# Kernel tuning notes

Measured on AMD Instinct MI355X. Metric: run time of the kernel, lower is better.

The kernel has to match this reference:

```python
import jax, jax.numpy as jnp
import numpy as np

B, T, D, H, L, F, V, BANDS = 16, 512, 1024, 8, 6, 4096, 30000, 16
RES = [1, 1, 2, 2, 4, 4, 8, 8]  # per-head K/V resolution schedule
HD = D // H


def setup_inputs() -> dict:
    key = jax.random.key(0)
    ks = iter(jax.random.split(key, 64))
    s = 0.02
    p = {
        "tokens": jax.random.randint(next(ks), (B, T), 0, V, dtype=jnp.int32),
        "embed": jax.random.normal(next(ks), (V, D), jnp.float32) * s,
        "pos_embed": jax.random.normal(next(ks), (T, D), jnp.float32) * s,
        "Wq": jax.random.normal(next(ks), (L, D, D), jnp.float32) * s,
        "bq": jnp.zeros((L, D), jnp.float32),
        "Wk": jax.random.normal(next(ks), (L, D, D), jnp.float32) * s,
        "bk": jnp.zeros((L, D), jnp.float32),
        "Wv": jax.random.normal(next(ks), (L, D, D), jnp.float32) * s,
        "bv": jnp.zeros((L, D), jnp.float32),
        "Wo": jax.random.normal(next(ks), (L, D, D), jnp.float32) * s,
        "bo": jnp.zeros((L, D), jnp.float32),
        "ln1_g": jnp.ones((L, D), jnp.float32),
        "ln1_b": jnp.zeros((L, D), jnp.float32),
        "ln2_g": jnp.ones((L, D), jnp.float32),
        "ln2_b": jnp.zeros((L, D), jnp.float32),
        "W1": jax.random.normal(next(ks), (L, D, F), jnp.float32) * s,
        "b1": jnp.zeros((L, F), jnp.float32),
        "W2": jax.random.normal(next(ks), (L, F, D), jnp.float32) * s,
        "b2": jnp.zeros((L, D), jnp.float32),
        "gates": jnp.ones((L, H, BANDS), jnp.float32),
        "lnf_g": jnp.ones((D,), jnp.float32),
        "lnf_b": jnp.zeros((D,), jnp.float32),
    }
    return p


def _ln(x, g, b, eps=1e-5):
    mu = jnp.mean(x, -1, keepdims=True)
    var = jnp.var(x, -1, keepdims=True)
    return (x - mu) * jax.lax.rsqrt(var + eps) * g + b


def _hfa_attention(x, Wq, bq, Wk, bk, Wv, bv, Wo, bo, gates_l):
    # x: [B,T,D]; per-head resolution schedule + spectral band gating.
    q = (x @ Wq + bq).reshape(B, T, H, HD).transpose(0, 2, 1, 3)  # [B,H,T,HD]
    k = (x @ Wk + bk).reshape(B, T, H, HD).transpose(0, 2, 1, 3)
    v = (x @ Wv + bv).reshape(B, T, H, HD).transpose(0, 2, 1, 3)
    nb = T // 2 + 1
    band_of_bin = (jnp.arange(nb) * BANDS) // nb  # map rfft bin -> spectral band
    scale = 1.0 / np.sqrt(HD)
    outs = []
    for h in range(H):
        r = RES[h]
        kh = k[:, h].reshape(B, T // r, r, HD).mean(2)  # pooled keys [B,T/r,HD]
        vh = v[:, h].reshape(B, T // r, r, HD).mean(2)
        scores = jnp.einsum("btd,bsd->bts", q[:, h], kh) * scale
        attn = jax.nn.softmax(scores, axis=-1)
        o = jnp.einsum("bts,bsd->btd", attn, vh)  # [B,T,HD]
        # spectral band gating along sequence axis
        g = gates_l[h][band_of_bin]  # [nb]
        f = jnp.fft.rfft(o, axis=1) * g[None, :, None]
        o = jnp.fft.irfft(f, n=T, axis=1)
        outs.append(o)
    out = jnp.concatenate(outs, axis=-1)  # [B,T,D]
    return out @ Wo + bo


def reference(tokens, embed, pos_embed, Wq, bq, Wk, bk, Wv, bv, Wo, bo,
              ln1_g, ln1_b, ln2_g, ln2_b, W1, b1, W2, b2, gates, lnf_g, lnf_b):
    x = embed[tokens] + pos_embed[jnp.arange(T)][None, :, :]  # [B,T,D]
    for l in range(L):
        h = _ln(x, ln1_g[l], ln1_b[l])
        x = x + _hfa_attention(h, Wq[l], bq[l], Wk[l], bk[l], Wv[l], bv[l],
                               Wo[l], bo[l], gates[l])
        h = _ln(x, ln2_g[l], ln2_b[l])
        ff = jax.nn.gelu(h @ W1[l] + b1[l], approximate=False) @ W2[l] + b2[l]
        x = x + ff
    return _ln(x, lnf_g, lnf_b)
```

## Files before the change

### kernel.cpp

```cpp
#include <hip/hip_runtime.h>
#include <hip/hip_bf16.h>
#include <math.h>

#define Bn 16
#define Tn 512
#define Dn 1024
#define Hn 8
#define Ln 6
#define Fn 4096
#define HDn 128

typedef __attribute__((ext_vector_type(8))) short short8;
typedef __attribute__((ext_vector_type(4))) float f32x4;

__device__ __forceinline__ float bf2f(unsigned short u){
  union{float f; unsigned int i;} c; c.i = ((unsigned int)u)<<16; return c.f;
}
__device__ __forceinline__ unsigned short f2bf(float f){
  union{float f; unsigned int i;} c; c.f=f;
  unsigned int r = c.i + 0x7fffu + ((c.i>>16)&1u);
  return (unsigned short)(r>>16);
}

#define GLOAD(gp, lp) __builtin_amdgcn_global_load_lds( \
    (const __attribute__((address_space(1))) void*)(const void*)(gp), \
    (__attribute__((address_space(3))) void*)(void*)(lp), 16, 0, 0)

__global__ __launch_bounds__(256) void embed_kernel(
    const int* __restrict__ tok, const float* __restrict__ emb,
    const float* __restrict__ pos, float* __restrict__ x){
  long row = blockIdx.x;
  int t = (int)(row & (Tn-1));
  int tk = tok[row];
  int d = threadIdx.x*4;
  float4 e = *(const float4*)(emb + (long)tk*Dn + d);
  float4 p = *(const float4*)(pos + (long)t*Dn + d);
  float4 r; r.x=e.x+p.x; r.y=e.y+p.y; r.z=e.z+p.z; r.w=e.w+p.w;
  *(float4*)(x + row*(long)Dn + d) = r;
}

template<int OUTBF>
__global__ __launch_bounds__(256) void ln_kernel(
    const float* __restrict__ x, const float* __restrict__ g,
    const float* __restrict__ b, void* __restrict__ outp){
  long row = blockIdx.x;
  const float* xr = x + row*(long)Dn;
  int tid = threadIdx.x;
  float4 v4 = *(const float4*)(xr + tid*4);
  float s  = v4.x+v4.y+v4.z+v4.w;
  float s2 = v4.x*v4.x + v4.y*v4.y + v4.z*v4.z + v4.w*v4.w;
  #pragma unroll
  for (int o=32;o;o>>=1){ s += __shfl_xor(s,o); s2 += __shfl_xor(s2,o); }
  __shared__ float rs[4], rs2[4];
  int w = tid>>6;
  if ((tid&63)==0){ rs[w]=s; rs2[w]=s2; }
  __syncthreads();
  s  = rs[0]+rs[1]+rs[2]+rs[3];
  s2 = rs2[0]+rs2[1]+rs2[2]+rs2[3];
  float mu  = s*(1.f/Dn);
  float var = s2*(1.f/Dn) - mu*mu;
  float rstd = rsqrtf(var + 1e-5f);
  float4 gg = *(const float4*)(g + tid*4);
  float4 bb = *(const float4*)(b + tid*4);
  float o0 = (v4.x-mu)*rstd*gg.x + bb.x;
  float o1 = (v4.y-mu)*rstd*gg.y + bb.y;
  float o2 = (v4.z-mu)*rstd*gg.z + bb.z;
  float o3 = (v4.w-mu)*rstd*gg.w + bb.w;
  if (OUTBF){
    unsigned short* o = (unsigned short*)outp + row*(long)Dn + tid*4;
    o[0]=f2bf(o0); o[1]=f2bf(o1); o[2]=f2bf(o2); o[3]=f2bf(o3);
  } else {
    float* o = (float*)outp + row*(long)Dn + tid*4;
    o[0]=o0; o[1]=o1; o[2]=o2; o[3]=o3;
  }
}

__global__ __launch_bounds__(256) void transpose_w(
    const float* __restrict__ W, unsigned short* __restrict__ WT, int Kd, int Nd){
  __shared__ float tile[32][33];
  long lofs = (long)blockIdx.z * Kd * Nd;
  int n0 = blockIdx.x*32, k0 = blockIdx.y*32;
  int tx = threadIdx.x & 31, ty = threadIdx.x >> 5;
  #pragma unroll
  for (int i=0;i<4;i++){
    int kk = k0 + ty + i*8;
    tile[ty+i*8][tx] = W[lofs + (long)kk*Nd + n0 + tx];
  }
  __syncthreads();
  #pragma unroll
  for (int i=0;i<4;i++){
    int nn = n0 + ty + i*8;
    WT[lofs + (long)nn*Kd + k0 + tx] = f2bf(tile[tx][ty+i*8]);
  }
}

__global__ __launch_bounds__(256) void pack_bias(
    const float* __restrict__ bq, const float* __restrict__ bk,
    const float* __restrict__ bv, float* __restrict__ bqkv){
  int i = blockIdx.x*256 + threadIdx.x;
  int l = i / (3*Dn); int r = i - l*3*Dn; int w = r / Dn; int d = r - w*Dn;
  const float* src = (w==0)? bq : ((w==1)? bk : bv);
  bqkv[i] = src[l*Dn + d];
}

__global__ __launch_bounds__(512) void ckern(
    const float* __restrict__ gates, float* __restrict__ cbuf){
  int lh = blockIdx.x;
  __shared__ float gb[16];
  if (threadIdx.x < 16) gb[threadIdx.x] = gates[lh*16 + threadIdx.x];
  __syncthreads();
  int m = threadIdx.x;
  float acc = gb[0];
  for (int j=1;j<256;j++){
    int band = (j*16)/257;
    int kmod = (j*m) & 511;
    acc += 2.f*gb[band]*cosf(1.2271846303085129e-2f * (float)kmod);
  }
  acc += gb[15] * ((m & 1) ? -1.f : 1.f);
  cbuf[lh*512 + m] = acc * (1.f/512.f);
}

__global__ __launch_bounds__(256) void gfill(
    const float* __restrict__ cbuf, unsigned short* __restrict__ G){
  long idx = (long)blockIdx.x*256 + threadIdx.x;
  int lh = (int)(idx >> 18);
  int rem = (int)(idx & 262143);
  int t = rem >> 9, s = rem & 511;
  G[idx] = f2bf(cbuf[lh*512 + ((t - s) & 511)]);
}

__global__ __launch_bounds__(256) void pool_kernel(
    const unsigned short* __restrict__ kin, const unsigned short* __restrict__ vin,
    unsigned short* __restrict__ kp, unsigned short* __restrict__ vTp){
  long idx = (long)blockIdx.x*256 + threadIdx.x;
  if (idx >= (long)Bn*1920*HDn) return;
  long rem = idx; int hh = 0; int S = 512;
  for (hh=0; hh<8; hh++){
    S = 512 >> (hh>>1);
    long seg = (long)Bn*S*HDn;
    if (rem < seg) break;
    rem -= seg;
  }
  int r = 512 / S;
  int d = (int)(rem % HDn);
  long t2 = rem / HDn;
  int s = (int)(t2 % S);
  int b = (int)(t2 / S);
  const unsigned short* kb = kin + ((long)(b*Tn + s*r))*Dn + hh*HDn + d;
  const unsigned short* vb = vin + ((long)(b*Tn + s*r))*Dn + hh*HDn + d;
  float ks=0.f, vs=0.f;
  for (int j=0;j<r;j++){ ks += bf2f(kb[(long)j*Dn]); vs += bf2f(vb[(long)j*Dn]); }
  float inv = 1.f/(float)r;
  int pref=0;
  for (int g2=0; g2<hh; g2++) pref += 512 >> (g2>>1);
  long segb = (long)Bn*HDn*pref;
  kp [segb + ((long)b*S + s)*HDn + d] = f2bf(ks*inv);
  vTp[segb + ((long)b*HDn + d)*S + s] = f2bf(vs*inv);
}

template<int S>
__global__ __launch_bounds__(256) void softmax_kernel(
    const float* __restrict__ sc, unsigned short* __restrict__ at){
  const int NV = S/64;
  long row = (long)blockIdx.x*4 + (threadIdx.x >> 6);
  const float* r = sc + row*(long)S;
  int lane = threadIdx.x & 63;
  float vals[NV];
  float mx = -1e30f;
  #pragma unroll
  for (int i=0;i<NV;i++){ vals[i] = r[lane + i*64] * 0.08838834764831845f; mx = fmaxf(mx, vals[i]); }
  #pragma unroll
  for (int o=32;o;o>>=1) mx = fmaxf(mx, __shfl_xor(mx, o));
  float sum = 0.f;
  #pragma unroll
  for (int i=0;i<NV;i++){ vals[i] = expf(vals[i]-mx); sum += vals[i]; }
  #pragma unroll
  for (int o=32;o;o>>=1) sum += __shfl_xor(sum, o);
  float inv = 1.f/sum;
  #pragma unroll
  for (int i=0;i<NV;i++) at[row*(long)S + lane + i*64] = f2bf(vals[i]*inv);
}

template<int MODE>
__global__ __launch_bounds__(256)
void gemm_kernel(const unsigned short* __restrict__ A, int lda, long sAb, long sAh,
                 const unsigned short* __restrict__ Bt, int ldb, long sBb, long sBh,
                 void* __restrict__ Cout, int ldc, long sCb, long sCh,
                 const float* __restrict__ bias, long sbias,
                 int zshift, int zmask,
                 int M, int N, int K)
{
  __shared__ unsigned short AB[2][2][128*64];
  int z = blockIdx.z;
  int zb = z & zmask, zh = z >> zshift;
  const unsigned short* Az = A + (long)zb*sAb + (long)zh*sAh;
  const unsigned short* Bz = Bt + (long)zb*sBb + (long)zh*sBh;
  const float* biasz = bias ? (bias + (long)zh*sbias) : nullptr;
  int m0 = blockIdx.y*128, n0 = blockIdx.x*128;
  int tid = threadIdx.x;
  int lane = tid & 63, wid = tid >> 6;
  int wm = wid >> 1, wn = wid & 1;
  f32x4 zero4 = {0.f,0.f,0.f,0.f};
  f32x4 acc[4][4];
  #pragma unroll
  for (int m=0;m<4;m++)
    #pragma unroll
    for (int n=0;n<4;n++)
      acc[m][n] = zero4;
  const int r16 = lane & 15, kq = lane >> 4;

  auto stage = [&](int buf, int k0){
    #pragma unroll
    for (int i=0;i<4;i++){
      int chunk = i*256 + tid;
      int row = chunk >> 3, c = chunk & 7;
      int cg = (c ^ (row & 7)) * 8;
      int gm = m0 + row; gm = gm < M ? gm : M-1;
      GLOAD(Az + (long)gm*lda + k0 + cg, AB[buf][0] + (i*256 + wid*64)*8);
    }
    #pragma unroll
    for (int i=0;i<4;i++){
      int chunk = i*256 + tid;
      int row = chunk >> 3, c = chunk & 7;
      int cg = (c ^ (row & 7)) * 8;
      int gn = n0 + row; gn = gn < N ? gn : N-1;
      GLOAD(Bz + (long)gn*ldb + k0 + cg, AB[buf][1] + (i*256 + wid*64)*8);
    }
  };

  int NT = K >> 6;
  stage(0, 0);
  for (int t = 0; t < NT; t++){
    if (t + 1 < NT){
      stage((t+1)&1, (t+1)*64);
      asm volatile("s_waitcnt vmcnt(8)" ::: "memory");
    } else {
      asm volatile("s_waitcnt vmcnt(0)" ::: "memory");
    }
    __builtin_amdgcn_s_barrier();
    const unsigned short* As = AB[t&1][0];
    const unsigned short* Bs = AB[t&1][1];
    #pragma unroll
    for (int kk=0; kk<64; kk+=32){
      short8 af[4], bfr[4];
      int kb = (kk + kq*8) * 2;
      #pragma unroll
      for (int m=0;m<4;m++){
        int row = wm*64 + m*16 + r16;
        af[m] = *(const short8*)((const char*)As + row*128 + (kb ^ ((row & 7) << 4)));
      }
      #pragma unroll
      for (int n=0;n<4;n++){
        int row = wn*64 + n*16 + r16;
        bfr[n] = *(const short8*)((const char*)Bs + row*128 + (kb ^ ((row & 7) << 4)));
      }
      #pragma unroll
      for (int m=0;m<4;m++)
        #pragma unroll
        for (int n=0;n<4;n++)
          acc[m][n] = __builtin_amdgcn_mfma_f32_16x16x32_bf16(af[m], bfr[n], acc[m][n], 0, 0, 0);
    }
    __builtin_amdgcn_s_barrier();
  }
  #pragma unroll
  for (int n=0;n<4;n++){
    int col = n0 + wn*64 + n*16 + r16;
    if (col >= N) continue;
    float bvv = 0.f;
    if (MODE != 0 && biasz != nullptr) bvv = biasz[col];
    #pragma unroll
    for (int m=0;m<4;m++){
      #pragma unroll
      for (int e=0;e<4;e++){
        int row = m0 + wm*64 + m*16 + kq*4 + e;
        if (row >= M) continue;
        float vv = acc[m][n][e] + bvv;
        long cidx = (long)zb*sCb + (long)zh*sCh + (long)row*ldc + col;
        if (MODE == 0)      ((float*)Cout)[cidx] = vv;
        else                ((unsigned short*)Cout)[cidx] = f2bf(vv);
      }
    }
  }
}

template<int MODE, int Mt, int Nt, int Kt, long SBH, long SCH, int BIASST>
__global__ __launch_bounds__(256)
void gemm_big(const unsigned short* __restrict__ A,
              const unsigned short* __restrict__ Bt,
              void* __restrict__ Cout,
              const float* __restrict__ bias)
{
  __shared__ char shraw[2][32768];
  int zh = blockIdx.z;
  const unsigned short* Bz = Bt + (long)zh*SBH;
  const float* biasz = bias + (long)zh*BIASST;
  int m0 = blockIdx.y*128, n0 = blockIdx.x*128;
  int tid = threadIdx.x;
  int lane = tid & 63, wid = tid >> 6;
  int wm = wid >> 1, wn = wid & 1;
  f32x4 zero4 = {0.f,0.f,0.f,0.f};
  f32x4 acc[4][4];
  #pragma unroll
  for (int m=0;m<4;m++)
    #pragma unroll
    for (int n=0;n<4;n++)
      acc[m][n] = zero4;
  const int r16 = lane & 15, kq = lane >> 4;

  const unsigned short* pA[4];
  const unsigned short* pB[4];
  #pragma unroll
  for (int i=0;i<4;i++){
    int chunk = i*256 + tid;
    int row = chunk >> 3, c = chunk & 7;
    int cg = (c ^ (row & 7)) * 8;
    pA[i] = A  + (long)(m0 + row)*Kt + cg;
    pB[i] = Bz + (long)(n0 + row)*Kt + cg;
  }
  auto stage = [&](int buf, int k0){
    unsigned short* As = (unsigned short*)shraw[buf];
    #pragma unroll
    for (int i=0;i<4;i++) GLOAD(pA[i] + k0, As + (i*256 + wid*64)*8);
    #pragma unroll
    for (int i=0;i<4;i++) GLOAD(pB[i] + k0, As + 8192 + (i*256 + wid*64)*8);
  };

  constexpr int NT = Kt/64;
  stage(0, 0);
  for (int t = 0; t < NT; t++){
    if (t + 1 < NT){
      stage((t+1)&1, (t+1)*64);
      asm volatile("s_waitcnt vmcnt(8)" ::: "memory");
    } else {
      asm volatile("s_waitcnt vmcnt(0)" ::: "memory");
    }
    __builtin_amdgcn_s_barrier();
    const unsigned short* As = (const unsigned short*)shraw[t&1];
    const unsigned short* Bs = As + 8192;
    #pragma unroll
    for (int kk=0; kk<64; kk+=32){
      short8 af[4], bfr[4];
      int kb = (kk + kq*8) * 2;
      #pragma unroll
      for (int m=0;m<4;m++){
        int row = wm*64 + m*16 + r16;
        af[m] = *(const short8*)((const char*)As + row*128 + (kb ^ ((row & 7) << 4)));
      }
      #pragma unroll
      for (int n=0;n<4;n++){
        int row = wn*64 + n*16 + r16;
        bfr[n] = *(const short8*)((const char*)Bs + row*128 + (kb ^ ((row & 7) << 4)));
      }
      #pragma unroll
      for (int m=0;m<4;m++)
        #pragma unroll
        for (int n=0;n<4;n++)
          acc[m][n] = __builtin_amdgcn_mfma_f32_16x16x32_bf16(af[m], bfr[n], acc[m][n], 0, 0, 0);
    }
    __builtin_amdgcn_s_barrier();
  }

  if (MODE == 1 || MODE == 2){
    unsigned short* shb = (unsigned short*)&shraw[0][0];
    #pragma unroll
    for (int n=0;n<4;n++){
      int col = wn*64 + n*16 + r16;
      float bvv = biasz[n0 + col];
      #pragma unroll
      for (int m=0;m<4;m++){
        #pragma unroll
        for (int e=0;e<4;e++){
          int row = wm*64 + m*16 + kq*4 + e;
          float vv = acc[m][n][e] + bvv;
          if (MODE == 2) vv = 0.5f*vv*(1.f + erff(vv*0.7071067811865475f));
          shb[row*136 + col] = f2bf(vv);
        }
      }
    }
    __syncthreads();
    #pragma unroll
    for (int i=0;i<8;i++){
      int chunk = i*256 + tid;
      int row = chunk >> 4, col = (chunk & 15)*8;
      short8 vv8 = *(const short8*)(shb + row*136 + col);
      *(short8*)((unsigned short*)Cout + (long)zh*SCH +
                 (long)(m0 + row)*Nt + n0 + col) = vv8;
    }
  } else {
    float* shf = (float*)&shraw[0][0];
    #pragma unroll
    for (int ph=0; ph<2; ph++){
      __syncthreads();
      if (wm == ph){
        #pragma unroll
        for (int n=0;n<4;n++){
          int col = wn*64 + n*16 + r16;
          float bvv = biasz[n0 + col];
          #pragma unroll
          for (int m=0;m<4;m++){
            #pragma unroll
            for (int e=0;e<4;e++){
              int rl = m*16 + kq*4 + e;
              shf[rl*136 + col] = acc[m][n][e] + bvv;
            }
          }
        }
      }
      __syncthreads();
      #pragma unroll
      for (int i=0;i<8;i++){
        int chunk = i*256 + tid;
        int row = chunk >> 5, col = (chunk & 31)*4;
        float4 vv = *(const float4*)(shf + row*136 + col);
        float* cp = (float*)Cout + (long)(m0 + ph*64 + row)*Nt + n0 + col;
        float4 o = *(const float4*)cp;
        o.x += vv.x; o.y += vv.y; o.z += vv.z; o.w += vv.w;
        *(float4*)cp = o;
      }
    }
  }
}

extern "C" void kernel_launch(void* const* d_in, const int* in_sizes, int n_in,
                              void* d_out, int out_size, void* d_ws, size_t ws_size,
                              hipStream_t stream){
  const int*   tokens = (const int*)  d_in[0];
  const float* embedp = (const float*)d_in[1];
  const float* pos    = (const float*)d_in[2];
  const float* Wq  = (const float*)d_in[3];
  const float* bq  = (const float*)d_in[4];
  const float* Wk  = (const float*)d_in[5];
  const float* bk  = (const float*)d_in[6];
  const float* Wv  = (const float*)d_in[7];
  const float* bv  = (const float*)d_in[8];
  const float* Wo  = (const float*)d_in[9];
  const float* bo  = (const float*)d_in[10];
  const float* ln1g= (const float*)d_in[11];
  const float* ln1b= (const float*)d_in[12];
  const float* ln2g= (const float*)d_in[13];
  const float* ln2b= (const float*)d_in[14];
  const float* W1  = (const float*)d_in[15];
  const float* b1  = (const float*)d_in[16];
  const float* W2  = (const float*)d_in[17];
  const float* b2  = (const float*)d_in[18];
  const float* gates=(const float*)d_in[19];
  const float* lnfg= (const float*)d_in[20];
  const float* lnfb= (const float*)d_in[21];
  float* out = (float*)d_out;

  char* base = (char*)d_ws;
  size_t off = 0;
  auto take = [&](size_t bytes)->char*{
    char* p = base + off;
    off = (off + bytes + 255) & ~(size_t)255;
    return p;
  };
  unsigned short* WqT = (unsigned short*)take((size_t)Ln*Dn*Dn*2);
  unsigned short* WkT = (unsigned short*)take((size_t)Ln*Dn*Dn*2);
  unsigned short* WvT = (unsigned short*)take((size_t)Ln*Dn*Dn*2);
  unsigned short* WoT = (unsigned short*)take((size_t)Ln*Dn*Dn*2);
  unsigned short* W1T = (unsigned short*)take((size_t)Ln*Dn*Fn*2);
  unsigned short* W2T = (unsigned short*)take((size_t)Ln*Dn*Fn*2);
  unsigned short* G   = (unsigned short*)take((size_t)Ln*Hn*Tn*Tn*2);
  float*          cbuf= (float*)take((size_t)Ln*Hn*Tn*4);
  float*          bqkv= (float*)take((size_t)Ln*3*Dn*4);
  float*          x   = (float*)take((size_t)Bn*Tn*Dn*4);
  unsigned short* hbuf= (unsigned short*)take((size_t)Bn*Tn*Dn*2);
  unsigned short* q   = (unsigned short*)take((size_t)Bn*Tn*Dn*2);
  unsigned short* k   = (unsigned short*)take((size_t)Bn*Tn*Dn*2);
  unsigned short* v   = (unsigned short*)take((size_t)Bn*Tn*Dn*2);
  unsigned short* kp  = (unsigned short*)take((size_t)Bn*1920*HDn*2);
  unsigned short* vTp = (unsigned short*)take((size_t)Bn*1920*HDn*2);
  unsigned short* ao  = (unsigned short*)take((size_t)Bn*Tn*Dn*2);
  unsigned short* ff1 = (unsigned short*)take((size_t)Bn*Tn*Fn*2);
  if (off > ws_size) return;
  float*          scoresA = (float*)ff1;
  unsigned short* attnA   = (unsigned short*)(scoresA + (size_t)2*Bn*Tn*512);
  unsigned short* oT = k;

  transpose_w<<<dim3(Dn/32, Dn/32, Ln), 256, 0, stream>>>(Wq, WqT, Dn, Dn);
  transpose_w<<<dim3(Dn/32, Dn/32, Ln), 256, 0, stream>>>(Wk, WkT, Dn, Dn);
  transpose_w<<<dim3(Dn/32, Dn/32, Ln), 256, 0, stream>>>(Wv, WvT, Dn, Dn);
  transpose_w<<<dim3(Dn/32, Dn/32, Ln), 256, 0, stream>>>(Wo, WoT, Dn, Dn);
  transpose_w<<<dim3(Fn/32, Dn/32, Ln), 256, 0, stream>>>(W1, W1T, Dn, Fn);
  transpose_w<<<dim3(Dn/32, Fn/32, Ln), 256, 0, stream>>>(W2, W2T, Fn, Dn);
  pack_bias<<<(Ln*3*Dn)/256, 256, 0, stream>>>(bq, bk, bv, bqkv);
  ckern<<<Ln*Hn, 512, 0, stream>>>(gates, cbuf);
  gfill<<<(Ln*Hn*Tn*Tn)/256, 256, 0, stream>>>(cbuf, G);
  embed_kernel<<<Bn*Tn, 256, 0, stream>>>(tokens, embedp, pos, x);

  const int pref[8] = {0,512,1024,1280,1536,1664,1792,1856};
  const int MT = Bn*Tn;

  for (int l=0; l<Ln; l++){
    ln_kernel<1><<<MT, 256, 0, stream>>>(x, ln1g + l*Dn, ln1b + l*Dn, hbuf);
    gemm_big<1, 8192, Dn, Dn, (long)Ln*Dn*Dn, (long)Bn*Tn*Dn, Dn>
        <<<dim3(Dn/128, MT/128, 3), 256, 0, stream>>>(
        hbuf, WqT + (size_t)l*Dn*Dn, q, bqkv + (size_t)l*3*Dn);
    pool_kernel<<<((long)Bn*1920*HDn + 255)/256, 256, 0, stream>>>(k, v, kp, vTp);

    for (int g=0; g<4; g++){
      int h0 = 2*g;
      int S  = Tn >> g;
      long koff = (long)Bn*HDn*pref[h0];
      gemm_kernel<0><<<dim3((S+127)/128, Tn/128, 32), 256, 0, stream>>>(
          q + h0*HDn, Dn, (long)Tn*Dn, (long)HDn,
          kp + koff, HDn, (long)S*HDn, (long)Bn*HDn*S,
          scoresA, S, (long)Tn*S, (long)Bn*Tn*S,
          nullptr, 0L, 4, 15,
          Tn, S, HDn);
      switch (S){
        case 512: softmax_kernel<512><<<2*MT/4, 256, 0, stream>>>(scoresA, attnA); break;
        case 256: softmax_kernel<256><<<2*MT/4, 256, 0, stream>>>(scoresA, attnA); break;
        case 128: softmax_kernel<128><<<2*MT/4, 256, 0, stream>>>(scoresA, attnA); break;
        default:  softmax_kernel< 64><<<2*MT/4, 256, 0, stream>>>(scoresA, attnA); break;
      }
      gemm_kernel<1><<<dim3(Tn/128, HDn/128, 32), 256, 0, stream>>>(
          vTp + koff, S, (long)HDn*S, (long)Bn*HDn*S,
          attnA, S, (long)Tn*S, (long)Bn*Tn*S,
          oT + (size_t)h0*Bn*HDn*Tn, Tn, (long)HDn*Tn, (long)Bn*HDn*Tn,
          nullptr, 0L, 4, 15,
          HDn, Tn, S);
    }
    gemm_kernel<1><<<dim3(1, Tn/128, 128), 256, 0, stream>>>(
        G + (size_t)(l*Hn)*Tn*Tn, Tn, 0L, (long)Tn*Tn,
        oT, Tn, (long)HDn*Tn, (long)Bn*HDn*Tn,
        ao, Dn, (long)Tn*Dn, (long)HDn,
        nullptr, 0L, 4, 15,
        Tn, HDn, Tn);
    gemm_big<3, 8192, Dn, Dn, 0L, 0L, 0>
        <<<dim3(Dn/128, MT/128, 1), 256, 0, stream>>>(
        ao, WoT + (size_t)l*Dn*Dn, x, bo + l*Dn);
    ln_kernel<1><<<MT, 256, 0, stream>>>(x, ln2g + l*Dn, ln2b + l*Dn, hbuf);
    gemm_big<2, 8192, Fn, Dn, 0L, 0L, 0>
        <<<dim3(Fn/128, MT/128, 1), 256, 0, stream>>>(
        hbuf, W1T + (size_t)l*Dn*Fn, ff1, b1 + l*Fn);
    gemm_big<3, 8192, Dn, Fn, 0L, 0L, 0>
        <<<dim3(Dn/128, MT/128, 1), 256, 0, stream>>>(
        ff1, W2T + (size_t)l*Dn*Fn, x, b2 + l*Dn);
  }
  ln_kernel<0><<<MT, 256, 0, stream>>>(x, lnfg, lnfb, out);
}
```

Measured before the change: 3.118 ms.

## Batch all attention head groups into single scores, softmax and PV launches

Replaces the per-resolution-group loop of twelve launches (scores GEMM, softmax, PV GEMM for each of four groups) with three launches covering all eight heads. Each kernel derives its head's pooled length and buffer offset from blockIdx. Scores and attention probabilities are packed for all heads, with attention getting its own workspace allocation. Block-level work is now unbalanced across heads: blocks for short heads exit early or loop fewer K tiles. Scores blocks use a fixed 128-wide tile even when the pooled length is 64. The aim is to cut launch and tail overhead and fill the GPU better for the small-S heads.

```diff
diff --git a/kernel.cpp b/kernel.cpp
--- a/kernel.cpp
+++ b/kernel.cpp
@@ -20,6 +20,10 @@
   union{float f; unsigned int i;} c; c.f=f;
   unsigned int r = c.i + 0x7fffu + ((c.i>>16)&1u);
   return (unsigned short)(r>>16);
+}
+__device__ __forceinline__ int pref_of(int h){
+  int g = h >> 1;
+  return (2048 - (2048 >> g)) + (h & 1) * (512 >> g);
 }
 
 #define GLOAD(gp, lp) __builtin_amdgcn_global_load_lds( \
@@ -158,27 +162,38 @@
   vTp[segb + ((long)b*HDn + d)*S + s] = f2bf(vs*inv);
 }
 
-template<int S>
-__global__ __launch_bounds__(256) void softmax_kernel(
+__global__ __launch_bounds__(256) void softmax_all(
     const float* __restrict__ sc, unsigned short* __restrict__ at){
-  const int NV = S/64;
-  long row = (long)blockIdx.x*4 + (threadIdx.x >> 6);
-  const float* r = sc + row*(long)S;
+  long rid = (long)blockIdx.x*4 + (threadIdx.x >> 6);
+  int head = (int)(rid >> 13);
+  int rih  = (int)(rid & 8191);
+  int g = head >> 1;
+  int S = 512 >> g;
+  int NV = S >> 6;
+  long base = (long)Bn*Tn*pref_of(head) + (long)rih*S;
+  const float* r = sc + base;
   int lane = threadIdx.x & 63;
-  float vals[NV];
+  float vals[8];
   float mx = -1e30f;
   #pragma unroll
-  for (int i=0;i<NV;i++){ vals[i] = r[lane + i*64] * 0.08838834764831845f; mx = fmaxf(mx, vals[i]); }
+  for (int i=0;i<8;i++){
+    if (i < NV){ vals[i] = r[lane + i*64] * 0.08838834764831845f; mx = fmaxf(mx, vals[i]); }
+  }
   #pragma unroll
   for (int o=32;o;o>>=1) mx = fmaxf(mx, __shfl_xor(mx, o));
   float sum = 0.f;
   #pragma unroll
-  for (int i=0;i<NV;i++){ vals[i] = expf(vals[i]-mx); sum += vals[i]; }
+  for (int i=0;i<8;i++){
+    if (i < NV){ vals[i] = expf(vals[i]-mx); sum += vals[i]; }
+  }
   #pragma unroll
   for (int o=32;o;o>>=1) sum += __shfl_xor(sum, o);
   float inv = 1.f/sum;
-  #pragma unroll
-  for (int i=0;i<NV;i++) at[row*(long)S + lane + i*64] = f2bf(vals[i]*inv);
+  unsigned short* ab = at + base;
+  #pragma unroll
+  for (int i=0;i<8;i++){
+    if (i < NV) ab[lane + i*64] = f2bf(vals[i]*inv);
+  }
 }
 
 template<int MODE>
@@ -278,6 +293,191 @@
         long cidx = (long)zb*sCb + (long)zh*sCh + (long)row*ldc + col;
         if (MODE == 0)      ((float*)Cout)[cidx] = vv;
         else                ((unsigned short*)Cout)[cidx] = f2bf(vv);
+      }
+    }
+  }
+}
+
+__global__ __launch_bounds__(256)
+void scores_all(const unsigned short* __restrict__ q,
+                const unsigned short* __restrict__ kp,
+                float* __restrict__ sc)
+{
+  __shared__ unsigned short AB[2][2][128*64];
+  int z = blockIdx.z;
+  int zb = z & 15, zh = z >> 4;
+  int g = zh >> 1;
+  int S = 512 >> g;
+  int n0 = blockIdx.x*128;
+  if (n0 >= S) return;
+  int pf = pref_of(zh);
+  const unsigned short* Az = q  + (long)zb*Tn*Dn + (long)zh*HDn;
+  const unsigned short* Bz = kp + (long)Bn*HDn*pf + (long)zb*S*HDn;
+  float* Cz = sc + (long)Bn*Tn*pf + (long)zb*Tn*S;
+  int m0 = blockIdx.y*128;
+  int tid = threadIdx.x;
+  int lane = tid & 63, wid = tid >> 6;
+  int wm = wid >> 1, wn = wid & 1;
+  f32x4 zero4 = {0.f,0.f,0.f,0.f};
+  f32x4 acc[4][4];
+  #pragma unroll
+  for (int m=0;m<4;m++)
+    #pragma unroll
+    for (int n=0;n<4;n++)
+      acc[m][n] = zero4;
+  const int r16 = lane & 15, kq = lane >> 4;
+
+  auto stage = [&](int buf, int k0){
+    #pragma unroll
+    for (int i=0;i<4;i++){
+      int chunk = i*256 + tid;
+      int row = chunk >> 3, c = chunk & 7;
+      int cg = (c ^ (row & 7)) * 8;
+      GLOAD(Az + (long)(m0 + row)*Dn + k0 + cg, AB[buf][0] + (i*256 + wid*64)*8);
+    }
+    #pragma unroll
+    for (int i=0;i<4;i++){
+      int chunk = i*256 + tid;
+      int row = chunk >> 3, c = chunk & 7;
+      int cg = (c ^ (row & 7)) * 8;
+      int gn = n0 + row; gn = gn < S ? gn : S-1;
+      GLOAD(Bz + (long)gn*HDn + k0 + cg, AB[buf][1] + (i*256 + wid*64)*8);
+    }
+  };
+
+  stage(0, 0);
+  stage(1, 64);
+  #pragma unroll
+  for (int t = 0; t < 2; t++){
+    if (t == 0) { asm volatile("s_waitcnt vmcnt(8)" ::: "memory"); }
+    else        { asm volatile("s_waitcnt vmcnt(0)" ::: "memory"); }
+    __builtin_amdgcn_s_barrier();
+    const unsigned short* As = AB[t][0];
+    const unsigned short* Bs = AB[t][1];
+    #pragma unroll
+    for (int kk=0; kk<64; kk+=32){
+      short8 af[4], bfr[4];
+      int kb = (kk + kq*8) * 2;
+      #pragma unroll
+      for (int m=0;m<4;m++){
+        int row = wm*64 + m*16 + r16;
+        af[m] = *(const short8*)((const char*)As + row*128 + (kb ^ ((row & 7) << 4)));
+      }
+      #pragma unroll
+      for (int n=0;n<4;n++){
+        int row = wn*64 + n*16 + r16;
+        bfr[n] = *(const short8*)((const char*)Bs + row*128 + (kb ^ ((row & 7) << 4)));
+      }
+      #pragma unroll
+      for (int m=0;m<4;m++)
+        #pragma unroll
+        for (int n=0;n<4;n++)
+          acc[m][n] = __builtin_amdgcn_mfma_f32_16x16x32_bf16(af[m], bfr[n], acc[m][n], 0, 0, 0);
+    }
+    __builtin_amdgcn_s_barrier();
+  }
+  #pragma unroll
+  for (int n=0;n<4;n++){
+    int col = n0 + wn*64 + n*16 + r16;
+    if (col >= S) continue;
+    #pragma unroll
+    for (int m=0;m<4;m++){
+      #pragma unroll
+      for (int e=0;e<4;e++){
+        int row = m0 + wm*64 + m*16 + kq*4 + e;
+        Cz[(long)row*S + col] = acc[m][n][e];
+      }
+    }
+  }
+}
+
+__global__ __launch_bounds__(256)
+void pv_all(const unsigned short* __restrict__ vTp,
+            const unsigned short* __restrict__ at,
+            unsigned short* __restrict__ oT)
+{
+  __shared__ unsigned short AB[2][2][128*64];
+  int z = blockIdx.z;
+  int zb = z & 15, zh = z >> 4;
+  int g = zh >> 1;
+  int S = 512 >> g;
+  int pf = pref_of(zh);
+  const unsigned short* Az = vTp + (long)Bn*HDn*pf + (long)zb*HDn*S;
+  const unsigned short* Bz = at  + (long)Bn*Tn*pf  + (long)zb*Tn*S;
+  unsigned short* Cz = oT + (long)zh*Bn*HDn*Tn + (long)zb*HDn*Tn;
+  int n0 = blockIdx.x*128;
+  int tid = threadIdx.x;
+  int lane = tid & 63, wid = tid >> 6;
+  int wm = wid >> 1, wn = wid & 1;
+  f32x4 zero4 = {0.f,0.f,0.f,0.f};
+  f32x4 acc[4][4];
+  #pragma unroll
+  for (int m=0;m<4;m++)
+    #pragma unroll
+    for (int n=0;n<4;n++)
+      acc[m][n] = zero4;
+  const int r16 = lane & 15, kq = lane >> 4;
+
+  auto stage = [&](int buf, int k0){
+    #pragma unroll
+    for (int i=0;i<4;i++){
+      int chunk = i*256 + tid;
+      int row = chunk >> 3, c = chunk & 7;
+      int cg = (c ^ (row & 7)) * 8;
+      GLOAD(Az + (long)row*S + k0 + cg, AB[buf][0] + (i*256 + wid*64)*8);
+    }
+    #pragma unroll
+    for (int i=0;i<4;i++){
+      int chunk = i*256 + tid;
+      int row = chunk >> 3, c = chunk & 7;
+      int cg = (c ^ (row & 7)) * 8;
+      GLOAD(Bz + (long)(n0 + row)*S + k0 + cg, AB[buf][1] + (i*256 + wid*64)*8);
+    }
+  };
+
+  int NT = S >> 6;
+  stage(0, 0);
+  for (int t = 0; t < NT; t++){
+    if (t + 1 < NT){
+      stage((t+1)&1, (t+1)*64);
+      asm volatile("s_waitcnt vmcnt(8)" ::: "memory");
+    } else {
+      asm volatile("s_waitcnt vmcnt(0)" ::: "memory");
+    }
+    __builtin_amdgcn_s_barrier();
+    const unsigned short* As = AB[t&1][0];
+    const unsigned short* Bs = AB[t&1][1];
+    #pragma unroll
+    for (int kk=0; kk<64; kk+=32){
+      short8 af[4], bfr[4];
+      int kb = (kk + kq*8) * 2;
+      #pragma unroll
+      for (int m=0;m<4;m++){
+        int row = wm*64 + m*16 + r16;
+        af[m] = *(const short8*)((const char*)As + row*128 + (kb ^ ((row & 7) << 4)));
+      }
+      #pragma unroll
+      for (int n=0;n<4;n++){
+        int row = wn*64 + n*16 + r16;
+        bfr[n] = *(const short8*)((const char*)Bs + row*128 + (kb ^ ((row & 7) << 4)));
+      }
+      #pragma unroll
+      for (int m=0;m<4;m++)
+        #pragma unroll
+        for (int n=0;n<4;n++)
+          acc[m][n] = __builtin_amdgcn_mfma_f32_16x16x32_bf16(af[m], bfr[n], acc[m][n], 0, 0, 0);
+    }
+    __builtin_amdgcn_s_barrier();
+  }
+  #pragma unroll
+  for (int n=0;n<4;n++){
+    int col = n0 + wn*64 + n*16 + r16;
+    #pragma unroll
+    for (int m=0;m<4;m++){
+      #pragma unroll
+      for (int e=0;e<4;e++){
+        int row = wm*64 + m*16 + kq*4 + e;
+        Cz[(long)row*Tn + col] = f2bf(acc[m][n][e]);
       }
     }
   }
@@ -473,9 +673,9 @@
   unsigned short* vTp = (unsigned short*)take((size_t)Bn*1920*HDn*2);
   unsigned short* ao  = (unsigned short*)take((size_t)Bn*Tn*Dn*2);
   unsigned short* ff1 = (unsigned short*)take((size_t)Bn*Tn*Fn*2);
+  unsigned short* attnA = (unsigned short*)take((size_t)Bn*1920*Tn*2);
   if (off > ws_size) return;
-  float*          scoresA = (float*)ff1;
-  unsigned short* attnA   = (unsigned short*)(scoresA + (size_t)2*Bn*Tn*512);
+  float* scoresA = (float*)ff1;
   unsigned short* oT = k;
 
   transpose_w<<<dim3(Dn/32, Dn/32, Ln), 256, 0, stream>>>(Wq, WqT, Dn, Dn);
@@ -489,7 +689,6 @@
   gfill<<<(Ln*Hn*Tn*Tn)/256, 256, 0, stream>>>(cbuf, G);
   embed_kernel<<<Bn*Tn, 256, 0, stream>>>(tokens, embedp, pos, x);
 
-  const int pref[8] = {0,512,1024,1280,1536,1664,1792,1856};
   const int MT = Bn*Tn;
 
   for (int l=0; l<Ln; l++){
@@ -499,29 +698,10 @@
         hbuf, WqT + (size_t)l*Dn*Dn, q, bqkv + (size_t)l*3*Dn);
     pool_kernel<<<((long)Bn*1920*HDn + 255)/256, 256, 0, stream>>>(k, v, kp, vTp);
 
-    for (int g=0; g<4; g++){
-      int h0 = 2*g;
-      int S  = Tn >> g;
-      long koff = (long)Bn*HDn*pref[h0];
-      gemm_kernel<0><<<dim3((S+127)/128, Tn/128, 32), 256, 0, stream>>>(
-          q + h0*HDn, Dn, (long)Tn*Dn, (long)HDn,
-          kp + koff, HDn, (long)S*HDn, (long)Bn*HDn*S,
-          scoresA, S, (long)Tn*S, (long)Bn*Tn*S,
-          nullptr, 0L, 4, 15,
-          Tn, S, HDn);
-      switch (S){
-        case 512: softmax_kernel<512><<<2*MT/4, 256, 0, stream>>>(scoresA, attnA); break;
-        case 256: softmax_kernel<256><<<2*MT/4, 256, 0, stream>>>(scoresA, attnA); break;
-        case 128: softmax_kernel<128><<<2*MT/4, 256, 0, stream>>>(scoresA, attnA); break;
-        default:  softmax_kernel< 64><<<2*MT/4, 256, 0, stream>>>(scoresA, attnA); break;
-      }
-      gemm_kernel<1><<<dim3(Tn/128, HDn/128, 32), 256, 0, stream>>>(
-          vTp + koff, S, (long)HDn*S, (long)Bn*HDn*S,
-          attnA, S, (long)Tn*S, (long)Bn*Tn*S,
-          oT + (size_t)h0*Bn*HDn*Tn, Tn, (long)HDn*Tn, (long)Bn*HDn*Tn,
-          nullptr, 0L, 4, 15,
-          HDn, Tn, S);
-    }
+    scores_all<<<dim3(4, Tn/128, 128), 256, 0, stream>>>(q, kp, scoresA);
+    softmax_all<<<(8*MT)/4, 256, 0, stream>>>(scoresA, attnA);
+    pv_all<<<dim3(Tn/128, 1, 128), 256, 0, stream>>>(vTp, attnA, oT);
+
     gemm_kernel<1><<<dim3(1, Tn/128, 128), 256, 0, stream>>>(
         G + (size_t)(l*Hn)*Tn*Tn, Tn, 0L, (long)Tn*Tn,
         oT, Tn, (long)HDn*Tn, (long)Bn*HDn*Tn,
```

Measured after the change: 2.877 ms. 7.7% less time.
